# Kernel optimization log

Measured on AMD Instinct MI355X. Metric: run time of the kernel, lower is better.

Reference implementation:

```python
import jax, jax.numpy as jnp
import numpy as np

W_DIM = 72  # positional_encoding(3 coords, 12 freqs) -> 3*12*2
_F1 = np.array([1.0, 3.0, 3.0, 1.0], dtype=np.float32)
_F2 = np.outer(_F1, _F1); _F2 = _F2 / _F2.sum()  # normalized StyleGAN resample filter


def upsample2x(x):
    """Antialiased 2x upsample: zero-insertion + 4-tap [1,3,3,1] FIR, gain=4 (upfirdn2d)."""
    C = x.shape[1]
    k = jnp.tile(jnp.asarray(_F2 * 4.0, x.dtype)[None, None], (C, 1, 1, 1))  # [C,1,4,4]
    return jax.lax.conv_general_dilated(
        x, k, (1, 1), ((2, 2), (2, 2)), lhs_dilation=(2, 2),
        feature_group_count=C, dimension_numbers=('NCHW', 'OIHW', 'NCHW'))


def affine(w_vec, aw, ab):
    # FullyConnectedLayer: runtime weight gain 1/sqrt(w_dim), bias init 1
    return (w_vec @ aw.T) / np.sqrt(W_DIM) + ab


def mod_conv(x, weight, styles, demodulate=True, padding=1):
    """StyleGAN2 modulated conv2d (batch=1). weight [Co,Ci,k,k], styles [Ci]."""
    w = weight * styles[None, :, None, None]
    if demodulate:
        d = jax.lax.rsqrt(jnp.sum(w * w, axis=(1, 2, 3)) + 1e-8)
        w = w * d[:, None, None, None]
    return jax.lax.conv_general_dilated(
        x, w, (1, 1), ((padding, padding), (padding, padding)),
        dimension_numbers=('NCHW', 'OIHW', 'NCHW'))


def syn_layer(x, w_vec, aw, ab, cw, cb, up):
    s = affine(w_vec, aw, ab)
    if up:
        x = upsample2x(x)
    x = mod_conv(x, cw, s, True, 1)
    # bias_act: lrelu, gain sqrt(2), conv_clamp 256 (noise_strength init 0 -> no noise)
    x = jax.nn.leaky_relu(x + cb[None, :, None, None], 0.2) * np.sqrt(2.0)
    return jnp.clip(x, -256.0, 256.0)


def to_rgb(x, w_vec, aw, ab, cw, cb):
    s = affine(w_vec, aw, ab) / np.sqrt(cw.shape[1])  # ToRGB weight_gain 1/sqrt(Cin)
    y = mod_conv(x, cw, s, False, 0)
    return jnp.clip(y + cb[None, :, None, None], -256.0, 256.0)


def reference(rays, rgbs, conv_w, conv_b, bn_gamma, bn_beta, bn_mean, bn_var,
              a0_w, a0_b, w0, b0, a1_w, a1_b, w1, b1, t0_aw, t0_ab, t0_w, t0_b,
              a2_w, a2_b, w2, b2, a3_w, a3_b, w3, b3, t1_aw, t1_ab, t1_w, t1_b):
    # style vector from positional encoding of ray origin
    p = rays[0, :3, 0, 0]
    fb = 2.0 ** jnp.arange(12, dtype=rays.dtype)
    pts = (p[:, None] * fb[None, :]).reshape(-1)  # (36,)
    w_vec = jnp.concatenate([jnp.sin(pts), jnp.cos(pts)])  # (72,)
    # mapping: 1x1 conv + relu + BatchNorm2d (eval-mode)
    feat = jnp.einsum('oi,bihw->bohw', conv_w[:, :, 0, 0], rgbs) + conv_b[None, :, None, None]
    feat = jax.nn.relu(feat)
    inv = jax.lax.rsqrt(bn_var + 1e-5)
    feat = (feat - bn_mean[None, :, None, None]) * (inv * bn_gamma)[None, :, None, None] + bn_beta[None, :, None, None]
    rgb = feat[:, :3]
    # block0: 32ch@128 -> 256ch@256, skip-architecture ToRGB
    x = syn_layer(feat, w_vec, a0_w, a0_b, w0, b0, True)
    x = syn_layer(x, w_vec, a1_w, a1_b, w1, b1, False)
    img = upsample2x(rgb) + to_rgb(x, w_vec, t0_aw, t0_ab, t0_w, t0_b)
    # block1: 256ch@256 -> 128ch@512
    x = syn_layer(x, w_vec, a2_w, a2_b, w2, b2, True)
    x = syn_layer(x, w_vec, a3_w, a3_b, w3, b3, False)
    img = upsample2x(img) + to_rgb(x, w_vec, t1_aw, t1_ab, t1_w, t1_b)
    return img  # [1,3,512,512]


def setup_inputs() -> dict:
    key = jax.random.key(0)
    ks = jax.random.split(key, 16)
    rn = lambda k, s: jax.random.normal(k, s, dtype=jnp.float32)
    z = lambda s: jnp.zeros(s, jnp.float32)
    o = lambda s: jnp.ones(s, jnp.float32)
    inp = {}
    inp['rays'] = rn(ks[0], (1, 6, 128, 128))
    inp['rgbs'] = jax.random.uniform(ks[1], (1, 3, 128, 128), dtype=jnp.float32)
    inp['conv_w'] = rn(ks[2], (32, 3, 1, 1)); inp['conv_b'] = z((32,))
    inp['bn_gamma'] = o((32,)); inp['bn_beta'] = z((32,))
    inp['bn_mean'] = z((32,)); inp['bn_var'] = o((32,))
    inp['a0_w'] = rn(ks[3], (32, 72)); inp['a0_b'] = o((32,))
    inp['w0'] = rn(ks[4], (256, 32, 3, 3)); inp['b0'] = z((256,))
    inp['a1_w'] = rn(ks[5], (256, 72)); inp['a1_b'] = o((256,))
    inp['w1'] = rn(ks[6], (256, 256, 3, 3)); inp['b1'] = z((256,))
    inp['t0_aw'] = rn(ks[7], (256, 72)); inp['t0_ab'] = o((256,))
    inp['t0_w'] = rn(ks[8], (3, 256, 1, 1)); inp['t0_b'] = z((3,))
    inp['a2_w'] = rn(ks[9], (256, 72)); inp['a2_b'] = o((256,))
    inp['w2'] = rn(ks[10], (128, 256, 3, 3)); inp['b2'] = z((128,))
    inp['a3_w'] = rn(ks[11], (128, 72)); inp['a3_b'] = o((128,))
    inp['w3'] = rn(ks[12], (128, 128, 3, 3)); inp['b3'] = z((128,))
    inp['t1_aw'] = rn(ks[13], (128, 72)); inp['t1_ab'] = o((128,))
    inp['t1_w'] = rn(ks[14], (3, 128, 1, 1)); inp['t1_b'] = z((3,))
    return inp
```

## Files before the change

### kernel.cpp

```cpp
#include <hip/hip_runtime.h>
#include <cstddef>

typedef __attribute__((ext_vector_type(8))) short short8;
typedef __attribute__((ext_vector_type(4))) float f32x4;
typedef __attribute__((address_space(3))) void lds_void;
typedef const __attribute__((address_space(1))) void glob_void;

static const size_t OFF_S0    = 0;
static const size_t OFF_S1    = 64;
static const size_t OFF_S2    = 320;
static const size_t OFF_S3    = 576;
static const size_t OFF_MT0   = 704;
static const size_t OFF_MT1   = 1472;
static const size_t OFF_ZERO  = 1856;
static const size_t OFF_RGBF  = 2048;
static const size_t OFF_IMG0  = 51200;
static const size_t OFF_RGBP  = 247808;
static const size_t OFF_WQ0   = 1900544;
static const size_t OFF_WQ1   = 1937408;
static const size_t OFF_WQ2   = 2232320;
static const size_t OFF_WQ3   = 2379776;
static const size_t OFF_FEAT  = 2453504;
static const size_t OFF_UFEAT = 2715648;
static const size_t OFF_X1    = 4194304;
static const size_t OFF_X2    = 4194304;
static const size_t OFF_U     = 20971520;
static const size_t OFF_X0    = 20971520;

__device__ __forceinline__ unsigned short f2bf(float f) {
  unsigned int u = __float_as_uint(f);
  return (unsigned short)((u + 0x7FFFu + ((u >> 16) & 1u)) >> 16);
}
__device__ __forceinline__ float b2f(short h) {
  return __uint_as_float(((unsigned int)(unsigned short)h) << 16);
}

__global__ void __launch_bounds__(256) prep_kernel(
    const float* __restrict__ rays,
    const float* __restrict__ a0w, const float* __restrict__ a0b,
    const float* __restrict__ a1w, const float* __restrict__ a1b,
    const float* __restrict__ t0aw, const float* __restrict__ t0ab,
    const float* __restrict__ a2w, const float* __restrict__ a2b,
    const float* __restrict__ a3w, const float* __restrict__ a3b,
    const float* __restrict__ t1aw, const float* __restrict__ t1ab,
    const float* __restrict__ t0w, const float* __restrict__ t1w,
    float* __restrict__ ws)
{
  __shared__ float wv[72];
  __shared__ float st0l[256];
  __shared__ float st1l[128];
  const int tid = threadIdx.x;
  if (tid < 128) ws[OFF_ZERO + tid] = 0.f;
  if (tid < 36) {
    int i = tid / 12, j = tid % 12;
    float v = rays[i * 16384] * (float)(1 << j);
    wv[tid]      = sinf(v);
    wv[36 + tid] = cosf(v);
  }
  __syncthreads();
  const float inv72 = 0.11785113019775793f;

  if (tid < 32) {
    float d = 0.f;
    for (int k = 0; k < 72; ++k) d += wv[k] * a0w[tid * 72 + k];
    ws[OFF_S0 + tid] = fmaf(d, inv72, a0b[tid]);
  }
  {
    float d = 0.f;
    for (int k = 0; k < 72; ++k) d += wv[k] * a1w[tid * 72 + k];
    ws[OFF_S1 + tid] = fmaf(d, inv72, a1b[tid]);
  }
  {
    float d = 0.f;
    for (int k = 0; k < 72; ++k) d += wv[k] * t0aw[tid * 72 + k];
    st0l[tid] = fmaf(d, inv72, t0ab[tid]) * 0.0625f;
  }
  {
    float d = 0.f;
    for (int k = 0; k < 72; ++k) d += wv[k] * a2w[tid * 72 + k];
    ws[OFF_S2 + tid] = fmaf(d, inv72, a2b[tid]);
  }
  if (tid < 128) {
    float d = 0.f;
    for (int k = 0; k < 72; ++k) d += wv[k] * a3w[tid * 72 + k];
    ws[OFF_S3 + tid] = fmaf(d, inv72, a3b[tid]);
  }
  if (tid < 128) {
    float d = 0.f;
    for (int k = 0; k < 72; ++k) d += wv[k] * t1aw[tid * 72 + k];
    st1l[tid] = fmaf(d, inv72, t1ab[tid]) * 0.08838834764831845f;
  }
  __syncthreads();
  for (int i = tid; i < 768; i += 256) ws[OFF_MT0 + i] = t0w[i] * st0l[i & 255];
  for (int i = tid; i < 384; i += 256) ws[OFF_MT1 + i] = t1w[i] * st1l[i & 127];
}

__global__ void __launch_bounds__(256) modw_kernel(
    const float* __restrict__ w, const float* __restrict__ s,
    unsigned short* __restrict__ wq, int Ci, int Co)
{
  const int co = blockIdx.x;
  const int n = Ci * 9;
  float local = 0.f;
  for (int i = threadIdx.x; i < n; i += 256) {
    float v = w[co * n + i] * s[i / 9];
    local += v * v;
  }
#pragma unroll
  for (int off = 32; off >= 1; off >>= 1) local += __shfl_xor(local, off);
  __shared__ float red[4];
  if ((threadIdx.x & 63) == 0) red[threadIdx.x >> 6] = local;
  __syncthreads();
  const float d = rsqrtf(red[0] + red[1] + red[2] + red[3] + 1e-8f);
  const int sxor = (co & 3) ^ ((co >> 2) & 3);
  for (int i = threadIdx.x; i < n; i += 256) {
    int ci = i / 9, t = i - ci * 9;
    int kk = ci & 31;
    int sl = (kk >> 3) ^ sxor;
    wq[(((size_t)(ci >> 5) * 9 + t) * Co + co) * 32 + (sl << 3) + (kk & 7)] =
        f2bf(w[co * n + i] * s[ci] * d);
  }
}

__global__ void __launch_bounds__(256) feat_kernel(
    const float* __restrict__ rgbs, const float* __restrict__ cw, const float* __restrict__ cb,
    const float* __restrict__ gam, const float* __restrict__ bet,
    const float* __restrict__ mean, const float* __restrict__ var,
    unsigned short* __restrict__ feat, float* __restrict__ rgbf)
{
  const int p = blockIdx.x * 256 + threadIdx.x;
  const float r = rgbs[p], g = rgbs[16384 + p], b = rgbs[32768 + p];
  unsigned int pk[16];
#pragma unroll
  for (int co = 0; co < 32; ++co) {
    float v = cw[co * 3] * r + cw[co * 3 + 1] * g + cw[co * 3 + 2] * b + cb[co];
    v = fmaxf(v, 0.f);
    float inv = rsqrtf(var[co] + 1e-5f);
    v = (v - mean[co]) * (inv * gam[co]) + bet[co];
    if (co < 3) rgbf[co * 16384 + p] = v;
    unsigned int h = f2bf(v);
    if ((co & 1) == 0) pk[co >> 1] = h;
    else               pk[co >> 1] |= h << 16;
  }
  uint4* dst = reinterpret_cast<uint4*>(feat + (size_t)p * 32);
#pragma unroll
  for (int q = 0; q < 4; ++q)
    dst[q] = make_uint4(pk[q * 4], pk[q * 4 + 1], pk[q * 4 + 2], pk[q * 4 + 3]);
}

__global__ void __launch_bounds__(256) up2x_nhwc_kernel(
    const unsigned short* __restrict__ in, unsigned short* __restrict__ out,
    int H, int W, int c8s , int w2s )
{
  const int cid = blockIdx.x * 256 + threadIdx.x;
  const int k = cid & ((1 << c8s) - 1);
  const int pix = cid >> c8s;
  const int ey = pix >> w2s;
  const int ex = pix & ((1 << w2s) - 1);
  const int C = 8 << c8s;
  int ry0; float ay0, ay1;
  if (ey & 1) { ry0 = ey >> 1;       ay0 = 0.75f; ay1 = 0.25f; }
  else        { ry0 = (ey >> 1) - 1; ay0 = 0.25f; ay1 = 0.75f; }
  int cx0; float bx0, bx1;
  if (ex & 1) { cx0 = ex >> 1;       bx0 = 0.75f; bx1 = 0.25f; }
  else        { cx0 = (ex >> 1) - 1; bx0 = 0.25f; bx1 = 0.75f; }
  const short8 z = {0, 0, 0, 0, 0, 0, 0, 0};
  short8 v00 = z, v01 = z, v10 = z, v11 = z;
  const bool yo0 = (ry0 >= 0), yo1 = (ry0 + 1 < H);
  const bool xo0 = (cx0 >= 0), xo1 = (cx0 + 1 < W);
  if (yo0 && xo0) v00 = *reinterpret_cast<const short8*>(in + ((size_t)(ry0 * W + cx0) * C + k * 8));
  if (yo0 && xo1) v01 = *reinterpret_cast<const short8*>(in + ((size_t)(ry0 * W + cx0 + 1) * C + k * 8));
  if (yo1 && xo0) v10 = *reinterpret_cast<const short8*>(in + ((size_t)((ry0 + 1) * W + cx0) * C + k * 8));
  if (yo1 && xo1) v11 = *reinterpret_cast<const short8*>(in + ((size_t)((ry0 + 1) * W + cx0 + 1) * C + k * 8));
  unsigned int o[4];
#pragma unroll
  for (int j = 0; j < 8; ++j) {
    float f = ay0 * (bx0 * b2f(v00[j]) + bx1 * b2f(v01[j]))
            + ay1 * (bx0 * b2f(v10[j]) + bx1 * b2f(v11[j]));
    unsigned int h = f2bf(f);
    if ((j & 1) == 0) o[j >> 1] = h;
    else              o[j >> 1] |= h << 16;
  }
  *reinterpret_cast<uint4*>(out + (size_t)pix * C + k * 8) = make_uint4(o[0], o[1], o[2], o[3]);
}

template <bool FUSE_RGB>
__global__ void __launch_bounds__(512) conv3x3_mfma(
    const unsigned short* __restrict__ in,
    const unsigned short* __restrict__ wq,
    const float* __restrict__ bias,
    unsigned short* __restrict__ out,
    const float* __restrict__ rgbw,
    float* __restrict__ rgbp,
    const unsigned short* __restrict__ zpage,
    int H, int W, int Ci, int Co)
{
  const int tid  = threadIdx.x;
  const int lane = tid & 63;
  const int wv   = tid >> 6;
  const int wr   = wv & 3;
  const int wg   = wv >> 2;
  const int lo   = lane & 15, hi = lane >> 4;
  const int tpr  = W >> 4;
  const int T_y  = (blockIdx.x / tpr) << 5;
  const int T_x  = (blockIdx.x % tpr) << 4;
  const int cogB = blockIdx.y << 7;
  const int cog  = cogB + (wg << 6);

  __shared__ short8 xs[2][2560];
  __shared__ short8 wlds[3][1536];
  __shared__ float  rw[FUSE_RGB ? 384 : 4];

  if (FUSE_RGB) {
    for (int i = tid; i < 3 * Co; i += 512) rw[i] = rgbw[i];
  }

  f32x4 acc[4][8];
#pragma unroll
  for (int a = 0; a < 4; ++a)
#pragma unroll
    for (int b = 0; b < 8; ++b) acc[a][b] = (f32x4){0.f, 0.f, 0.f, 0.f};

  const unsigned short* gsrc[5];
#pragma unroll
  for (int j = 0; j < 5; ++j) {
    const int s = j * 512 + tid;
    const int pix = s >> 2, kslot = s & 3;
    const int rr = pix / 18, cc = pix - rr * 18;
    const int gy = T_y - 1 + rr, gx = T_x - 1 + cc;
    const int k = kslot ^ ((cc >> 1) & 3);
    const bool inb = (s < 2448) && gy >= 0 && gy < H && gx >= 0 && gx < W;
    gsrc[j] = inb ? (in + ((size_t)(gy * W + gx) * Ci + (k << 3))) : zpage;
  }

#define STAGE(c, buf)                                                              \
  {                                                                                \
    const int cb_ = (c) << 5;                                                      \
    _Pragma("unroll")                                                              \
    for (int j = 0; j < 5; ++j)                                                    \
      __builtin_amdgcn_global_load_lds((glob_void*)(gsrc[j] + cb_),                \
                                       (lds_void*)&xs[buf][j * 512 + tid], 16, 0, 0); \
  }

#define STAGE_W(C, KX, BUF)                                                        \
  {                                                                                \
    _Pragma("unroll")                                                              \
    for (int j = 0; j < 3; ++j) {                                                  \
      const unsigned short* src_ =                                                 \
          wq + ((size_t)((C) * 9 + j * 3 + (KX)) * Co + cogB) * 32 + tid * 8;      \
      __builtin_amdgcn_global_load_lds((glob_void*)src_,                           \
                                       (lds_void*)&wlds[BUF][(j << 9) + tid], 16, 0, 0); \
    }                                                                              \
  }

  const int sxa   = (lo & 3) ^ ((lo >> 2) & 3);
  const int wbase = (((wg << 6) + lo) << 2) + (hi ^ sxa);
#define ALOADW(SLOT, KY, BUF)                                                      \
  {                                                                                \
    _Pragma("unroll")                                                              \
    for (int cf = 0; cf < 4; ++cf)                                                 \
      apf[SLOT][cf] = wlds[BUF][((KY) << 9) + wbase + (cf << 6)];                  \
  }

#define MF(A, B, C) __builtin_amdgcn_mfma_f32_16x16x32_bf16(A, B, C, 0, 0, 0)

#define COMPUTE_GROUP(G)                                                           \
  {                                                                                \
    const int tx2  = lo + (G);                                                     \
    const int xv_  = hi ^ ((tx2 >> 1) & 3);                                        \
    const int rowb = (((wr << 3) * 18 + tx2) << 2) + xv_;                          \
    short8 q0 = xs[cur][rowb];                                                     \
    short8 q1 = xs[cur][rowb + 72];                                                \
    short8 q2 = xs[cur][rowb + 2 * 72];                                            \
    short8 q3 = xs[cur][rowb + 3 * 72];                                            \
    short8 q4 = xs[cur][rowb + 4 * 72];                                            \
    short8 q5 = xs[cur][rowb + 5 * 72];                                            \
    short8 q6 = xs[cur][rowb + 6 * 72];                                            \
    short8 q7 = xs[cur][rowb + 7 * 72];                                            \
    short8 apf[2][4];                                                              \
    ALOADW(0, 0, G);                                                               \
    ALOADW(1, 1, G);                                                               \
    __builtin_amdgcn_s_setprio(1);                                                 \
    _Pragma("unroll")                                                              \
    for (int cf = 0; cf < 4; ++cf) {                                               \
      acc[cf][0] = MF(apf[0][cf], q0, acc[cf][0]);                                 \
      acc[cf][1] = MF(apf[0][cf], q1, acc[cf][1]);                                 \
      acc[cf][2] = MF(apf[0][cf], q2, acc[cf][2]);                                 \
      acc[cf][3] = MF(apf[0][cf], q3, acc[cf][3]);                                 \
      acc[cf][4] = MF(apf[0][cf], q4, acc[cf][4]);                                 \
      acc[cf][5] = MF(apf[0][cf], q5, acc[cf][5]);                                 \
      acc[cf][6] = MF(apf[0][cf], q6, acc[cf][6]);                                 \
      acc[cf][7] = MF(apf[0][cf], q7, acc[cf][7]);                                 \
    }                                                                              \
    __builtin_amdgcn_s_setprio(0);                                                 \
    short8 q8 = xs[cur][rowb + 8 * 72];                                            \
    ALOADW(0, 2, G);                                                               \
    __builtin_amdgcn_s_setprio(1);                                                 \
    _Pragma("unroll")                                                              \
    for (int cf = 0; cf < 4; ++cf) {                                               \
      acc[cf][0] = MF(apf[1][cf], q1, acc[cf][0]);                                 \
      acc[cf][1] = MF(apf[1][cf], q2, acc[cf][1]);                                 \
      acc[cf][2] = MF(apf[1][cf], q3, acc[cf][2]);                                 \
      acc[cf][3] = MF(apf[1][cf], q4, acc[cf][3]);                                 \
      acc[cf][4] = MF(apf[1][cf], q5, acc[cf][4]);                                 \
      acc[cf][5] = MF(apf[1][cf], q6, acc[cf][5]);                                 \
      acc[cf][6] = MF(apf[1][cf], q7, acc[cf][6]);                                 \
      acc[cf][7] = MF(apf[1][cf], q8, acc[cf][7]);                                 \
    }                                                                              \
    __builtin_amdgcn_s_setprio(0);                                                 \
    short8 q9 = xs[cur][rowb + 9 * 72];                                            \
    __builtin_amdgcn_s_setprio(1);                                                 \
    _Pragma("unroll")                                                              \
    for (int cf = 0; cf < 4; ++cf) {                                               \
      acc[cf][0] = MF(apf[0][cf], q2, acc[cf][0]);                                 \
      acc[cf][1] = MF(apf[0][cf], q3, acc[cf][1]);                                 \
      acc[cf][2] = MF(apf[0][cf], q4, acc[cf][2]);                                 \
      acc[cf][3] = MF(apf[0][cf], q5, acc[cf][3]);                                 \
      acc[cf][4] = MF(apf[0][cf], q6, acc[cf][4]);                                 \
      acc[cf][5] = MF(apf[0][cf], q7, acc[cf][5]);                                 \
      acc[cf][6] = MF(apf[0][cf], q8, acc[cf][6]);                                 \
      acc[cf][7] = MF(apf[0][cf], q9, acc[cf][7]);                                 \
    }                                                                              \
    __builtin_amdgcn_s_setprio(0);                                                 \
  }

  STAGE(0, 0);
  STAGE_W(0, 0, 0);
  asm volatile("s_waitcnt vmcnt(0) lgkmcnt(0)" ::: "memory");
  __builtin_amdgcn_s_barrier();

  const int nch = Ci >> 5;
  for (int c = 0; c < nch; ++c) {
    const int cur = c & 1;
    const int cnext = (c + 1 < nch) ? (c + 1) : 0;

    STAGE_W(c, 1, 1);
    STAGE_W(c, 2, 2);
    STAGE(cnext, cur ^ 1);
    COMPUTE_GROUP(0)
    asm volatile("s_waitcnt vmcnt(8)" ::: "memory");
    __builtin_amdgcn_s_barrier();

    COMPUTE_GROUP(1)
    asm volatile("s_waitcnt vmcnt(5)" ::: "memory");
    __builtin_amdgcn_s_barrier();

    STAGE_W(cnext, 0, 0);
    COMPUTE_GROUP(2)
    asm volatile("s_waitcnt vmcnt(0)" ::: "memory");
    __builtin_amdgcn_s_barrier();
  }
#undef STAGE
#undef STAGE_W
#undef ALOADW
#undef MF
#undef COMPUTE_GROUP

  const float rt2 = 1.41421356237309515f;
#pragma unroll
  for (int r = 0; r < 8; ++r) {
    const int gy = T_y + (wr << 3) + r;
    const int gx = T_x + lo;
    if (!FUSE_RGB) {
#pragma unroll
      for (int cf = 0; cf < 4; ++cf) {
        const int cb = cog + (cf << 4) + (hi << 2);
        const f32x4 bi = *reinterpret_cast<const f32x4*>(bias + cb);
        unsigned short h[4];
#pragma unroll
        for (int reg = 0; reg < 4; ++reg) {
          float vv = acc[cf][r][reg] + bi[reg];
          vv = (vv >= 0.f) ? vv : 0.2f * vv;
          vv *= rt2;
          vv = fminf(fmaxf(vv, -256.f), 256.f);
          h[reg] = f2bf(vv);
        }
        uint2 pk;
        pk.x = (unsigned int)h[0] | ((unsigned int)h[1] << 16);
        pk.y = (unsigned int)h[2] | ((unsigned int)h[3] << 16);
        *reinterpret_cast<uint2*>(out + (size_t)(gy * W + gx) * Co + cb) = pk;
      }
    } else {
      float p0 = 0.f, p1 = 0.f, p2 = 0.f;
#pragma unroll
      for (int cf = 0; cf < 4; ++cf) {
        const int cb = cog + (cf << 4) + (hi << 2);
        const f32x4 bi = *reinterpret_cast<const f32x4*>(bias + cb);
#pragma unroll
        for (int reg = 0; reg < 4; ++reg) {
          float vv = acc[cf][r][reg] + bi[reg];
          vv = (vv >= 0.f) ? vv : 0.2f * vv;
          vv *= rt2;
          vv = fminf(fmaxf(vv, -256.f), 256.f);
          p0 = fmaf(rw[cb + reg], vv, p0);
          p1 = fmaf(rw[Co + cb + reg], vv, p1);
          p2 = fmaf(rw[2 * Co + cb + reg], vv, p2);
        }
      }
      p0 += __shfl_xor(p0, 16); p0 += __shfl_xor(p0, 32);
      p1 += __shfl_xor(p1, 16); p1 += __shfl_xor(p1, 32);
      p2 += __shfl_xor(p2, 16); p2 += __shfl_xor(p2, 32);
      if (hi == 0) {
        const size_t HWs = (size_t)H * W;
        const size_t px  = (size_t)gy * W + gx;
        rgbp[((size_t)wg * 3 + 0) * HWs + px] = p0;
        rgbp[((size_t)wg * 3 + 1) * HWs + px] = p1;
        rgbp[((size_t)wg * 3 + 2) * HWs + px] = p2;
      }
    }
  }
}

__device__ __forceinline__ float up2x_sample(const float* __restrict__ im, int H, int W,
                                             int oy, int ox)
{
  int my = oy >> 1, mx = ox >> 1;
  int ry0; float ay0, ay1;
  if (oy & 1) { ry0 = my;     ay0 = 0.75f; ay1 = 0.25f; }
  else        { ry0 = my - 1; ay0 = 0.25f; ay1 = 0.75f; }
  int cx0; float bx0, bx1;
  if (ox & 1) { cx0 = mx;     bx0 = 0.75f; bx1 = 0.25f; }
  else        { cx0 = mx - 1; bx0 = 0.25f; bx1 = 0.75f; }
  float v00 = (ry0 >= 0    && cx0 >= 0   ) ? im[ry0 * W + cx0]           : 0.f;
  float v01 = (ry0 >= 0    && cx0 + 1 < W) ? im[ry0 * W + cx0 + 1]       : 0.f;
  float v10 = (ry0 + 1 < H && cx0 >= 0   ) ? im[(ry0 + 1) * W + cx0]     : 0.f;
  float v11 = (ry0 + 1 < H && cx0 + 1 < W) ? im[(ry0 + 1) * W + cx0 + 1] : 0.f;
  return ay0 * (bx0 * v00 + bx1 * v01) + ay1 * (bx0 * v10 + bx1 * v11);
}

__global__ void __launch_bounds__(256) img0_kernel(
    const float* __restrict__ rgbf, const unsigned short* __restrict__ x1,
    const float* __restrict__ mt0g, const float* __restrict__ tb,
    float* __restrict__ img0)
{
  __shared__ float mt[768];
  const int tid = threadIdx.x;
  for (int i = tid; i < 768; i += 256) mt[i] = mt0g[i];
  __syncthreads();
  const int p = blockIdx.x * 256 + tid;
  const unsigned short* xp = x1 + (size_t)p * 256;
  float a0 = 0.f, a1 = 0.f, a2 = 0.f;
  for (int i8 = 0; i8 < 32; ++i8) {
    const short8 v = *reinterpret_cast<const short8*>(xp + i8 * 8);
#pragma unroll
    for (int j = 0; j < 8; ++j) {
      const float xv = b2f(v[j]);
      const int ci = i8 * 8 + j;
      a0 = fmaf(mt[ci],       xv, a0);
      a1 = fmaf(mt[256 + ci], xv, a1);
      a2 = fmaf(mt[512 + ci], xv, a2);
    }
  }
  const int oy = p >> 8, ox = p & 255;
  float av[3] = {a0, a1, a2};
#pragma unroll
  for (int o = 0; o < 3; ++o) {
    float y = fminf(fmaxf(av[o] + tb[o], -256.f), 256.f);
    img0[o * 65536 + p] = up2x_sample(rgbf + o * 16384, 128, 128, oy, ox) + y;
  }
}

__global__ void __launch_bounds__(256) final_kernel(
    const float* __restrict__ img0, const float* __restrict__ rgbp,
    const float* __restrict__ tb, float* __restrict__ out)
{
  const int p = blockIdx.x * 256 + threadIdx.x;
  const int oy = p >> 9, ox = p & 511;
#pragma unroll
  for (int o = 0; o < 3; ++o) {
    float a = rgbp[(0 * 3 + o) * 262144 + p] + rgbp[(1 * 3 + o) * 262144 + p];
    float y = fminf(fmaxf(a + tb[o], -256.f), 256.f);
    out[o * 262144 + p] = up2x_sample(img0 + o * 65536, 256, 256, oy, ox) + y;
  }
}

extern "C" void kernel_launch(void* const* d_in, const int* in_sizes, int n_in,
                              void* d_out, int out_size, void* d_ws, size_t ws_size,
                              hipStream_t stream)
{
  const float* rays   = (const float*)d_in[0];
  const float* rgbs   = (const float*)d_in[1];
  const float* conv_w = (const float*)d_in[2];
  const float* conv_b = (const float*)d_in[3];
  const float* bn_g   = (const float*)d_in[4];
  const float* bn_b   = (const float*)d_in[5];
  const float* bn_m   = (const float*)d_in[6];
  const float* bn_v   = (const float*)d_in[7];
  const float* a0_w   = (const float*)d_in[8];
  const float* a0_b   = (const float*)d_in[9];
  const float* w0     = (const float*)d_in[10];
  const float* b0     = (const float*)d_in[11];
  const float* a1_w   = (const float*)d_in[12];
  const float* a1_b   = (const float*)d_in[13];
  const float* w1     = (const float*)d_in[14];
  const float* b1     = (const float*)d_in[15];
  const float* t0_aw  = (const float*)d_in[16];
  const float* t0_ab  = (const float*)d_in[17];
  const float* t0_w   = (const float*)d_in[18];
  const float* t0_b   = (const float*)d_in[19];
  const float* a2_w   = (const float*)d_in[20];
  const float* a2_b   = (const float*)d_in[21];
  const float* w2     = (const float*)d_in[22];
  const float* b2     = (const float*)d_in[23];
  const float* a3_w   = (const float*)d_in[24];
  const float* a3_b   = (const float*)d_in[25];
  const float* w3     = (const float*)d_in[26];
  const float* b3     = (const float*)d_in[27];
  const float* t1_aw  = (const float*)d_in[28];
  const float* t1_ab  = (const float*)d_in[29];
  const float* t1_w   = (const float*)d_in[30];
  const float* t1_b   = (const float*)d_in[31];

  float* ws  = (float*)d_ws;
  float* out = (float*)d_out;

  unsigned short* wq0   = (unsigned short*)(ws + OFF_WQ0);
  unsigned short* wq1   = (unsigned short*)(ws + OFF_WQ1);
  unsigned short* wq2   = (unsigned short*)(ws + OFF_WQ2);
  unsigned short* wq3   = (unsigned short*)(ws + OFF_WQ3);
  unsigned short* featb = (unsigned short*)(ws + OFF_FEAT);
  unsigned short* ufeat = (unsigned short*)(ws + OFF_UFEAT);
  unsigned short* x0b   = (unsigned short*)(ws + OFF_X0);
  unsigned short* x1b   = (unsigned short*)(ws + OFF_X1);
  unsigned short* x2b   = (unsigned short*)(ws + OFF_X2);
  unsigned short* Ub    = (unsigned short*)(ws + OFF_U);
  const unsigned short* zpage = (const unsigned short*)(ws + OFF_ZERO);

  prep_kernel<<<1, 256, 0, stream>>>(rays, a0_w, a0_b, a1_w, a1_b, t0_aw, t0_ab,
                                     a2_w, a2_b, a3_w, a3_b, t1_aw, t1_ab,
                                     t0_w, t1_w, ws);
  modw_kernel<<<256, 256, 0, stream>>>(w0, ws + OFF_S0, wq0, 32, 256);
  modw_kernel<<<256, 256, 0, stream>>>(w1, ws + OFF_S1, wq1, 256, 256);
  modw_kernel<<<128, 256, 0, stream>>>(w2, ws + OFF_S2, wq2, 256, 128);
  modw_kernel<<<128, 256, 0, stream>>>(w3, ws + OFF_S3, wq3, 128, 128);
  feat_kernel<<<64, 256, 0, stream>>>(rgbs, conv_w, conv_b, bn_g, bn_b, bn_m, bn_v,
                                      featb, ws + OFF_RGBF);
  up2x_nhwc_kernel<<<1024, 256, 0, stream>>>(featb, ufeat, 128, 128, 2, 8);
  conv3x3_mfma<false><<<dim3(128, 2), 512, 0, stream>>>(
      ufeat, wq0, b0, x0b, nullptr, nullptr, zpage, 256, 256, 32, 256);
  conv3x3_mfma<false><<<dim3(128, 2), 512, 0, stream>>>(
      x0b, wq1, b1, x1b, nullptr, nullptr, zpage, 256, 256, 256, 256);
  img0_kernel<<<256, 256, 0, stream>>>(ws + OFF_RGBF, x1b, ws + OFF_MT0, t0_b,
                                       ws + OFF_IMG0);
  up2x_nhwc_kernel<<<32768, 256, 0, stream>>>(x1b, Ub, 256, 256, 5, 9);
  conv3x3_mfma<false><<<dim3(512, 1), 512, 0, stream>>>(
      Ub, wq2, b2, x2b, nullptr, nullptr, zpage, 512, 512, 256, 128);
  conv3x3_mfma<true><<<dim3(512, 1), 512, 0, stream>>>(
      x2b, wq3, b3, nullptr, ws + OFF_MT1, ws + OFF_RGBP, zpage, 512, 512, 128, 128);
  final_kernel<<<1024, 256, 0, stream>>>(ws + OFF_IMG0, ws + OFF_RGBP, t1_b, out);
}
```

Measured before the change: 406.7 us.

## Replace double/triple-buffered LDS staging with single-buffered serialized loads

Drops the double-buffered input tile and triple-buffered weight slices in the 3x3 conv kernel, so there is one buffer for each. Each compute group now waits at a barrier, issues its global-to-LDS load, and drains it fully before the next compute starts. This shrinks LDS use considerably, which may let more blocks run on each CU. In exchange it serializes memory transfer with MFMA compute and removes the prefetch overlap.

Result: slower. 431.5 us (+6.1%).

```diff
diff --git a/kernel.cpp b/kernel.cpp
--- a/kernel.cpp
+++ b/kernel.cpp
@@ -207,8 +207,8 @@
   const int cogB = blockIdx.y << 7;
   const int cog  = cogB + (wg << 6);
 
-  __shared__ short8 xs[2][2560];
-  __shared__ short8 wlds[3][1536];
+  __shared__ short8 xs[2560];
+  __shared__ short8 wl[1536];
   __shared__ float  rw[FUSE_RGB ? 384 : 4];
 
   if (FUSE_RGB) {
@@ -233,33 +233,33 @@
     gsrc[j] = inb ? (in + ((size_t)(gy * W + gx) * Ci + (k << 3))) : zpage;
   }
 
-#define STAGE(c, buf)                                                              \
+#define STAGE(c)                                                                   \
   {                                                                                \
     const int cb_ = (c) << 5;                                                      \
     _Pragma("unroll")                                                              \
     for (int j = 0; j < 5; ++j)                                                    \
       __builtin_amdgcn_global_load_lds((glob_void*)(gsrc[j] + cb_),                \
-                                       (lds_void*)&xs[buf][j * 512 + tid], 16, 0, 0); \
-  }
-
-#define STAGE_W(C, KX, BUF)                                                        \
+                                       (lds_void*)&xs[j * 512 + tid], 16, 0, 0);   \
+  }
+
+#define STAGE_W(C, KX)                                                             \
   {                                                                                \
     _Pragma("unroll")                                                              \
     for (int j = 0; j < 3; ++j) {                                                  \
       const unsigned short* src_ =                                                 \
           wq + ((size_t)((C) * 9 + j * 3 + (KX)) * Co + cogB) * 32 + tid * 8;      \
       __builtin_amdgcn_global_load_lds((glob_void*)src_,                           \
-                                       (lds_void*)&wlds[BUF][(j << 9) + tid], 16, 0, 0); \
+                                       (lds_void*)&wl[(j << 9) + tid], 16, 0, 0);  \
     }                                                                              \
   }
 
   const int sxa   = (lo & 3) ^ ((lo >> 2) & 3);
   const int wbase = (((wg << 6) + lo) << 2) + (hi ^ sxa);
-#define ALOADW(SLOT, KY, BUF)                                                      \
+#define ALOADW(SLOT, KY)                                                           \
   {                                                                                \
     _Pragma("unroll")                                                              \
     for (int cf = 0; cf < 4; ++cf)                                                 \
-      apf[SLOT][cf] = wlds[BUF][((KY) << 9) + wbase + (cf << 6)];                  \
+      apf[SLOT][cf] = wl[((KY) << 9) + wbase + (cf << 6)];                         \
   }
 
 #define MF(A, B, C) __builtin_amdgcn_mfma_f32_16x16x32_bf16(A, B, C, 0, 0, 0)
@@ -269,17 +269,17 @@
     const int tx2  = lo + (G);                                                     \
     const int xv_  = hi ^ ((tx2 >> 1) & 3);                                        \
     const int rowb = (((wr << 3) * 18 + tx2) << 2) + xv_;                          \
-    short8 q0 = xs[cur][rowb];                                                     \
-    short8 q1 = xs[cur][rowb + 72];                                                \
-    short8 q2 = xs[cur][rowb + 2 * 72];                                            \
-    short8 q3 = xs[cur][rowb + 3 * 72];                                            \
-    short8 q4 = xs[cur][rowb + 4 * 72];                                            \
-    short8 q5 = xs[cur][rowb + 5 * 72];                                            \
-    short8 q6 = xs[cur][rowb + 6 * 72];                                            \
-    short8 q7 = xs[cur][rowb + 7 * 72];                                            \
+    short8 q0 = xs[rowb];                                                          \
+    short8 q1 = xs[rowb + 72];                                                     \
+    short8 q2 = xs[rowb + 2 * 72];                                                 \
+    short8 q3 = xs[rowb + 3 * 72];                                                 \
+    short8 q4 = xs[rowb + 4 * 72];                                                 \
+    short8 q5 = xs[rowb + 5 * 72];                                                 \
+    short8 q6 = xs[rowb + 6 * 72];                                                 \
+    short8 q7 = xs[rowb + 7 * 72];                                                 \
     short8 apf[2][4];                                                              \
-    ALOADW(0, 0, G);                                                               \
-    ALOADW(1, 1, G);                                                               \
+    ALOADW(0, 0);                                                                  \
+    ALOADW(1, 1);                                                                  \
     __builtin_amdgcn_s_setprio(1);                                                 \
     _Pragma("unroll")                                                              \
     for (int cf = 0; cf < 4; ++cf) {                                               \
@@ -293,8 +293,8 @@
       acc[cf][7] = MF(apf[0][cf], q7, acc[cf][7]);                                 \
     }                                                                              \
     __builtin_amdgcn_s_setprio(0);                                                 \
-    short8 q8 = xs[cur][rowb + 8 * 72];                                            \
-    ALOADW(0, 2, G);                                                               \
+    short8 q8 = xs[rowb + 8 * 72];                                                 \
+    ALOADW(0, 2);                                                                  \
     __builtin_amdgcn_s_setprio(1);                                                 \
     _Pragma("unroll")                                                              \
     for (int cf = 0; cf < 4; ++cf) {                                               \
@@ -308,7 +308,7 @@
       acc[cf][7] = MF(apf[1][cf], q8, acc[cf][7]);                                 \
     }                                                                              \
     __builtin_amdgcn_s_setprio(0);                                                 \
-    short8 q9 = xs[cur][rowb + 9 * 72];                                            \
+    short8 q9 = xs[rowb + 9 * 72];                                                 \
     __builtin_amdgcn_s_setprio(1);                                                 \
     _Pragma("unroll")                                                              \
     for (int cf = 0; cf < 4; ++cf) {                                               \
@@ -324,37 +324,41 @@
     __builtin_amdgcn_s_setprio(0);                                                 \
   }
 
-  STAGE(0, 0);
-  STAGE_W(0, 0, 0);
+#define DRAIN_BAR                                                                  \
+  asm volatile("s_waitcnt vmcnt(0)" ::: "memory");                                 \
+  __builtin_amdgcn_s_barrier();
+
+  STAGE(0);
+  STAGE_W(0, 0);
   asm volatile("s_waitcnt vmcnt(0) lgkmcnt(0)" ::: "memory");
   __builtin_amdgcn_s_barrier();
 
   const int nch = Ci >> 5;
   for (int c = 0; c < nch; ++c) {
-    const int cur = c & 1;
-    const int cnext = (c + 1 < nch) ? (c + 1) : 0;
-
-    STAGE_W(c, 1, 1);
-    STAGE_W(c, 2, 2);
-    STAGE(cnext, cur ^ 1);
     COMPUTE_GROUP(0)
-    asm volatile("s_waitcnt vmcnt(8)" ::: "memory");
     __builtin_amdgcn_s_barrier();
+    STAGE_W(c, 1);
+    DRAIN_BAR
 
     COMPUTE_GROUP(1)
-    asm volatile("s_waitcnt vmcnt(5)" ::: "memory");
     __builtin_amdgcn_s_barrier();
-
-    STAGE_W(cnext, 0, 0);
+    STAGE_W(c, 2);
+    DRAIN_BAR
+
     COMPUTE_GROUP(2)
-    asm volatile("s_waitcnt vmcnt(0)" ::: "memory");
     __builtin_amdgcn_s_barrier();
+    if (c + 1 < nch) {
+      STAGE(c + 1);
+      STAGE_W(c + 1, 0);
+      DRAIN_BAR
+    }
   }
 #undef STAGE
 #undef STAGE_W
 #undef ALOADW
 #undef MF
 #undef COMPUTE_GROUP
+#undef DRAIN_BAR
 
   const float rt2 = 1.41421356237309515f;
 #pragma unroll
```
